# Optimization experiments

Hardware: AMD Instinct MI355X
Metric: run time of the kernel (lower is better)

The kernel has to match this reference:

```python
import jax, jax.numpy as jnp
import numpy as np

B, NPG, DIN, ED, DEG = 16, 1024, 16, 8, 32
HEADS, OUT1 = 5, 6
HID = HEADS * OUT1          # 30 features after conv1
C1, C2 = 32, 4              # DIFFPool cluster counts
N = B * NPG                 # 16384 total nodes
E = N * DEG                 # 524288 edges


def _egat_conv(x, src, dst, eattr, W, a_s, a_d, We, heads, outc, n_nodes):
    # Edge-gated GAT: per-edge attention logits from src/dst node features plus
    # a linear projection of edge attributes, segment-softmax over incoming edges.
    h = (x @ W).reshape(n_nodes, heads, outc)
    logit = jax.nn.leaky_relu((h[src] * a_s).sum(-1) + (h[dst] * a_d).sum(-1) + eattr @ We, 0.2)  # [E, heads]
    m = jax.ops.segment_max(logit, dst, num_segments=n_nodes)
    ex = jnp.exp(logit - m[dst])
    den = jax.ops.segment_sum(ex, dst, num_segments=n_nodes)
    alpha = ex / (den[dst] + 1e-16)
    out = jax.ops.segment_sum(alpha[:, :, None] * h[src], dst, num_segments=n_nodes)
    return out.reshape(n_nodes, heads * outc), alpha


def _diff_pool(x, adj, s_logits, b, n, c, d):
    s = jax.nn.softmax(s_logits.reshape(b, n, c), axis=-1)
    xp = jnp.einsum('bnc,bnd->bcd', s, x.reshape(b, n, d))
    adjp = jnp.einsum('bnc,bnm,bmk->bck', s, adj, s)
    reg = jnp.mean((adj - jnp.einsum('bnc,bmc->bnm', s, s)) ** 2)  # link-pred loss
    return xp.reshape(b * c, d), adjp, reg


def _dense_edges(b, c):
    base = jnp.arange(c)
    off = (jnp.arange(b) * c)[:, None]
    src = (jnp.repeat(base, c)[None, :] + off).reshape(-1)
    dst = (jnp.tile(base, c)[None, :] + off).reshape(-1)
    return src, dst


def _forward(x, edge_index, edge_attr, adj, params):
    (W1, a_src1, a_dst1, We1, Wp1, as_p1, ad_p1, Wep1,
     Wp2, as_p2, ad_p2, Wep2, Wf1, bf1, Wf2, bf2) = params
    src, dst = edge_index[0], edge_index[1]
    x1, e = _egat_conv(x, src, dst, edge_attr, W1, a_src1, a_dst1, We1, HEADS, OUT1, N)  # [N,30]
    e_dot = jnp.prod(e, axis=-1)[:, None]  # _EGATConv.dot: product over heads (unused downstream)
    s1, _ = _egat_conv(x1, src, dst, edge_attr, Wp1, as_p1, ad_p1, Wep1, 1, C1, N)
    x2, adj2, reg1 = _diff_pool(x1, adj, s1, B, NPG, C1, HID)
    src2, dst2 = _dense_edges(B, C1)
    ea2 = adj2.reshape(B * C1 * C1, 1)  # pooled graph is dense; adj values as edge attrs
    s2, _ = _egat_conv(x2, src2, dst2, ea2, Wp2, as_p2, ad_p2, Wep2, 1, C2, B * C1)
    x3, _, reg2 = _diff_pool(x2, adj2, s2, B, C1, C2, HID)
    reg = reg1 * 10.0 + reg2 * 0.1
    z = x3.reshape(B, C2 * HID)
    z = jax.nn.relu(z @ Wf1 + bf1)
    logits = z @ Wf2 + bf2
    return logits, reg


def setup_inputs() -> dict:
    key = jax.random.key(0)
    ks = jax.random.split(key, 20)
    # block-diagonal random edges: each graph has NPG*DEG edges within its block
    src_l = jax.random.randint(ks[0], (B, NPG * DEG), 0, NPG)
    dst_l = jax.random.randint(ks[1], (B, NPG * DEG), 0, NPG)
    off = (jnp.arange(B) * NPG)[:, None]
    edge_index = jnp.stack([(src_l + off).reshape(-1), (dst_l + off).reshape(-1)])
    adj = jnp.zeros((B, NPG, NPG), jnp.float32).at[jnp.arange(B)[:, None], src_l, dst_l].set(1.0)
    edge_attr = jax.random.uniform(ks[2], (E, ED), jnp.float32)
    x = jax.random.normal(ks[3], (N, DIN), jnp.float32)
    y = jax.random.randint(ks[4], (B,), 0, 2)

    def nrm(k, shape, fan):
        return jax.random.normal(k, shape, jnp.float32) / np.float32(np.sqrt(fan))

    return dict(
        x=x, edge_index=edge_index, edge_attr=edge_attr, y=y, adj=adj,
        W1=nrm(ks[5], (DIN, HEADS * OUT1), DIN),
        a_src1=nrm(ks[6], (HEADS, OUT1), OUT1),
        a_dst1=nrm(ks[7], (HEADS, OUT1), OUT1),
        We1=nrm(ks[8], (ED, HEADS), ED),
        Wp1=nrm(ks[9], (HID, C1), HID),
        as_p1=nrm(ks[10], (1, C1), C1),
        ad_p1=nrm(ks[11], (1, C1), C1),
        Wep1=nrm(ks[12], (ED, 1), ED),
        Wp2=nrm(ks[13], (HID, C2), HID),
        as_p2=nrm(ks[14], (1, C2), C2),
        ad_p2=nrm(ks[15], (1, C2), C2),
        Wep2=nrm(ks[16], (1, 1), 1),
        Wf1=nrm(ks[17], (C2 * HID, 32), C2 * HID),
        bf1=jnp.zeros((32,), jnp.float32),
        Wf2=nrm(ks[18], (32, 2), 32),
        bf2=jnp.zeros((2,), jnp.float32),
    )


def reference(x, edge_index, edge_attr, y, adj, W1, a_src1, a_dst1, We1, Wp1, as_p1, ad_p1, Wep1, Wp2, as_p2, ad_p2, Wep2, Wf1, bf1, Wf2, bf2):
    params = (W1, a_src1, a_dst1, We1, Wp1, as_p1, ad_p1, Wep1,
              Wp2, as_p2, ad_p2, Wep2, Wf1, bf1, Wf2, bf2)
    return _forward(x, edge_index, edge_attr, adj, params)
```

## Files before the change

kernel.cpp:

```cpp
#include <hip/hip_runtime.h>
#include <math.h>

#define NB 16
#define NPG 1024
#define DIN 16
#define ED 8
#define NHEADS 5
#define OUT1 6
#define HID 30
#define C1 32
#define C2 4
#define NN (NB*NPG)
#define EE (NN*32)
#define EPG 32768
#define CH 16
#define CE 2048

__device__ __forceinline__ float lrelu(float v){ return v >= 0.f ? v : 0.2f*v; }

__device__ __forceinline__ void chunk_gc(int& g, int& c){
    int x = blockIdx.x & 7;
    int j = blockIdx.x >> 3;
    g = x + 8*(j >> 4);
    c = j & 15;
}

__device__ __forceinline__ size_t xcd_chunk_base(){
    int x = blockIdx.x & 7;
    int j = blockIdx.x >> 3;
    int g = x + 8*(j >> 7);
    int c = j & 127;
    return (size_t)g*EPG + (size_t)c*256;
}

__global__ void k_hist_chunk(const int* __restrict__ src, const int* __restrict__ dst,
                             int* __restrict__ histD, int* __restrict__ histS,
                             const float* __restrict__ x, const float* __restrict__ W1,
                             const float* __restrict__ as1, const float* __restrict__ ad1,
                             float* __restrict__ h1, float* __restrict__ hs1, float* __restrict__ hd1){
    int t = threadIdx.x;
    if (blockIdx.x < 256){
        __shared__ int hD[NPG], hS[NPG];
        for (int i = t; i < NPG; i += 256){ hD[i] = 0; hS[i] = 0; }
        __syncthreads();
        int g, c; chunk_gc(g, c);
        size_t e0 = ((size_t)g*CH + c)*CE;
        #pragma unroll
        for (int i = 0; i < 8; i++){
            size_t e = e0 + i*256 + t;
            atomicAdd(&hD[dst[e] & (NPG-1)], 1);
            atomicAdd(&hS[src[e] & (NPG-1)], 1);
        }
        __syncthreads();
        size_t hb = ((size_t)g*CH + c)*NPG;
        for (int i = t; i < NPG; i += 256){
            histD[hb + i] = hD[i];
            histS[hb + i] = hS[i];
        }
        return;
    }
    __shared__ float Ws[DIN*HID];
    __shared__ float as_s[HID], ad_s[HID];
    for (int i = t; i < DIN*HID; i += blockDim.x) Ws[i] = W1[i];
    if (t < HID){ as_s[t] = as1[t]; ad_s[t] = ad1[t]; }
    __syncthreads();
    int n = (blockIdx.x - 256)*blockDim.x + t;
    if (n >= NN) return;
    float xv[DIN];
    #pragma unroll
    for (int i = 0; i < DIN; i++) xv[i] = x[n*DIN + i];
    float hv[HID];
    #pragma unroll
    for (int j = 0; j < HID; j++){
        float a = 0.f;
        #pragma unroll
        for (int i = 0; i < DIN; i++) a += xv[i]*Ws[i*HID + j];
        hv[j] = a; h1[(size_t)n*HID + j] = a;
    }
    #pragma unroll
    for (int h = 0; h < NHEADS; h++){
        float s = 0.f, d = 0.f;
        #pragma unroll
        for (int c2 = 0; c2 < OUT1; c2++){ s += hv[h*OUT1+c2]*as_s[h*OUT1+c2]; d += hv[h*OUT1+c2]*ad_s[h*OUT1+c2]; }
        hs1[n*NHEADS + h] = s; hd1[n*NHEADS + h] = d;
    }
}

__global__ __launch_bounds__(1024) void k_cumscan(int* __restrict__ histD, int* __restrict__ histS,
                                                  int* __restrict__ rowptr, int* __restrict__ rowptrS){
    __shared__ int wtot[16], wbase[16];
    bool isD = (blockIdx.x < NB);
    int b = isD ? blockIdx.x : (blockIdx.x - NB);
    int* hist = isD ? histD : histS;
    int* rp   = isD ? rowptr : rowptrS;
    int n = threadIdx.x;
    int run = 0;
    #pragma unroll
    for (int c = 0; c < CH; c++){
        size_t idx = ((size_t)b*CH + c)*NPG + n;
        int v = hist[idx];
        hist[idx] = run;
        run += v;
    }
    int lane = n & 63, wv = n >> 6;
    int sincl = run;
    #pragma unroll
    for (int off = 1; off < 64; off <<= 1){
        int v = __shfl_up(sincl, off, 64);
        if (lane >= off) sincl += v;
    }
    if (lane == 63) wtot[wv] = sincl;
    __syncthreads();
    if (n == 0){
        int r = 0;
        #pragma unroll
        for (int w = 0; w < 16; w++){ wbase[w] = r; r += wtot[w]; }
    }
    __syncthreads();
    int excl = wbase[wv] + sincl - run;
    rp[b*NPG + n] = b*EPG + excl;
    if (b == NB-1 && n == NPG-1) rp[NN] = EE;
}

__global__ void k_scatter_det(const int* __restrict__ src, const int* __restrict__ dst,
                              const int* __restrict__ rowptr, const int* __restrict__ rowptrS,
                              const int* __restrict__ histD, const int* __restrict__ histS,
                              int* __restrict__ srcs, int* __restrict__ eid,
                              int* __restrict__ dsts, int* __restrict__ nbrS){
    __shared__ int baseD[NPG], baseS[NPG];
    int t = threadIdx.x;
    int g, c; chunk_gc(g, c);
    size_t hb = ((size_t)g*CH + c)*NPG;
    for (int i = t; i < NPG; i += 256){
        baseD[i] = rowptr[g*NPG + i] + histD[hb + i];
        baseS[i] = rowptrS[g*NPG + i] + histS[hb + i];
    }
    __syncthreads();
    size_t e0 = ((size_t)g*CH + c)*CE;
    #pragma unroll
    for (int i = 0; i < 8; i++){
        size_t e = e0 + i*256 + t;
        int s = src[e], d = dst[e];
        int p = atomicAdd(&baseD[d & (NPG-1)], 1);
        srcs[p] = s; eid[p] = (int)e; dsts[p] = d;
        int pS = atomicAdd(&baseS[s & (NPG-1)], 1);
        nbrS[pS] = d;
    }
}

__global__ void k_elogit(const float* __restrict__ ea, const float* __restrict__ We1,
                         const float* __restrict__ Wep1,
                         const int* __restrict__ srcs, const int* __restrict__ eid,
                         const int* __restrict__ dsts,
                         const float* __restrict__ hs1, const float* __restrict__ hd1,
                         float* __restrict__ lg1T, float* __restrict__ ewp1s){
    __shared__ float W[ED*NHEADS];
    __shared__ float Wp[ED];
    int t = threadIdx.x;
    if (t < ED*NHEADS) W[t] = We1[t];
    if (t < ED) Wp[t] = Wep1[t];
    __syncthreads();
    size_t k = xcd_chunk_base() + t;
    int s = srcs[k], e = eid[k], d = dsts[k];
    float a[ED];
    #pragma unroll
    for (int i = 0; i < ED; i++) a[i] = ea[(size_t)e*ED + i];
    const float* hsr = hs1 + (size_t)s*NHEADS;
    const float* hdr = hd1 + (size_t)d*NHEADS;
    #pragma unroll
    for (int h = 0; h < NHEADS; h++){
        float sv = 0.f;
        #pragma unroll
        for (int i = 0; i < ED; i++) sv += a[i]*W[i*NHEADS + h];
        lg1T[(size_t)h*EE + k] = lrelu(hsr[h] + hdr[h] + sv);
    }
    float sv = 0.f;
    #pragma unroll
    for (int i = 0; i < ED; i++) sv += a[i]*Wp[i];
    ewp1s[k] = sv;
}

__global__ __launch_bounds__(640) void k_conv1_agg(const int* __restrict__ srcs,
                            const int* __restrict__ rowptr,
                            const float* __restrict__ h1, const float* __restrict__ lg1T,
                            float* __restrict__ x1){
    __shared__ float hls[NPG*HID];
    int t = threadIdx.x;
    int xx = blockIdx.x & 7;
    int j = blockIdx.x >> 3;
    int g = xx + 8*(j >> 4);
    int seg = j & 15;
    const float* hg = h1 + (size_t)g*NPG*HID;
    for (int i = t; i < NPG*HID; i += 640) hls[i] = hg[i];
    __syncthreads();
    int nl = seg*64 + t/10;
    int r = t - (t/10)*10;
    int h = r >> 1;
    int q = r & 1;
    int n = g*NPG + nl;
    int k0 = rowptr[n], k1 = rowptr[n+1];
    const float* lgh = lg1T + (size_t)h*EE;
    int off = h*OUT1 + q*3;
    float m = -INFINITY, den = 0.f;
    float acc[3] = {0.f, 0.f, 0.f};
    int k = k0;
    for (; k + 4 <= k1; k += 4){
        float l0 = lgh[k+0], l1 = lgh[k+1], l2 = lgh[k+2], l3 = lgh[k+3];
        int s0 = srcs[k+0] & (NPG-1), s1 = srcs[k+1] & (NPG-1);
        int s2 = srcs[k+2] & (NPG-1), s3 = srcs[k+3] & (NPG-1);
        const float* p0 = hls + s0*HID + off;
        const float* p1 = hls + s1*HID + off;
        const float* p2 = hls + s2*HID + off;
        const float* p3 = hls + s3*HID + off;
        float mb = fmaxf(fmaxf(l0, l1), fmaxf(l2, l3));
        float mn = fmaxf(m, mb);
        float f  = expf(m - mn);
        float e0 = expf(l0 - mn), e1 = expf(l1 - mn);
        float e2 = expf(l2 - mn), e3 = expf(l3 - mn);
        m = mn;
        den = den*f + e0 + e1 + e2 + e3;
        #pragma unroll
        for (int c = 0; c < 3; c++)
            acc[c] = acc[c]*f + e0*p0[c] + e1*p1[c] + e2*p2[c] + e3*p3[c];
    }
    for (; k < k1; k++){
        float l = lgh[k];
        int s = srcs[k] & (NPG-1);
        float mn = fmaxf(m, l);
        float f  = expf(m - mn);
        float ex = expf(l - mn);
        m = mn;
        den = den*f + ex;
        const float* hr = hls + s*HID + off;
        #pragma unroll
        for (int c = 0; c < 3; c++) acc[c] = acc[c]*f + ex*hr[c];
    }
    float inv = 1.f / (den + 1e-16f);
    #pragma unroll
    for (int c = 0; c < 3; c++) x1[(size_t)n*HID + off + c] = acc[c]*inv;
}

__global__ void k_pd(const float* __restrict__ x1, const float* __restrict__ Wp1,
                     const float* __restrict__ asp, const float* __restrict__ adp,
                     float* __restrict__ hp1, float* __restrict__ hsp, float* __restrict__ hdp,
                     const int* __restrict__ rowptrS, const int* __restrict__ nbrS,
                     int* __restrict__ unbr, int* __restrict__ ucnt,
                     float* __restrict__ scal){
    __shared__ float Ws[HID*C1];
    __shared__ float as_s[C1], ad_s[C1];
    __shared__ unsigned int bm[256*33];
    __shared__ int red[256];
    int t = threadIdx.x;
    if (blockIdx.x < 64){
        for (int i = t; i < HID*C1; i += blockDim.x) Ws[i] = Wp1[i];
        if (t < C1){ as_s[t] = asp[t]; ad_s[t] = adp[t]; }
        __syncthreads();
        int n = blockIdx.x*blockDim.x + t;
        float xv[HID];
        #pragma unroll
        for (int d = 0; d < HID; d++) xv[d] = x1[(size_t)n*HID + d];
        float s = 0.f, dd = 0.f;
        for (int c = 0; c < C1; c++){
            float a = 0.f;
            #pragma unroll
            for (int d = 0; d < HID; d++) a += xv[d]*Ws[d*C1 + c];
            hp1[(size_t)n*C1 + c] = a;
            s += a*as_s[c]; dd += a*ad_s[c];
        }
        hsp[n] = s; hdp[n] = dd;
        return;
    }
    unsigned int* mybm = &bm[t*33];
    #pragma unroll
    for (int i = 0; i < 32; i++) mybm[i] = 0u;
    int n = (blockIdx.x - 64)*blockDim.x + t;
    int cnt = 0;
    {
        int k0 = rowptrS[n], k1 = rowptrS[n+1];
        for (int k = k0; k < k1; k++){
            int m = nbrS[k];
            int loc = m & (NPG-1);
            unsigned int w = (unsigned int)(loc >> 5);
            unsigned int bit = 1u << (loc & 31);
            unsigned int old = mybm[w];
            if (!(old & bit)){
                mybm[w] = old | bit;
                unbr[k0 + cnt] = m;
                cnt++;
            }
        }
        ucnt[n] = cnt;
    }
    red[t] = cnt; __syncthreads();
    for (int s = 128; s > 0; s >>= 1){ if (t < s) red[t] += red[t+s]; __syncthreads(); }
    if (t == 0) atomicAdd(&scal[0], (float)red[0]);
}

__global__ void k_plogit(const int* __restrict__ srcs, const int* __restrict__ dsts,
                         const float* __restrict__ hsp, const float* __restrict__ hdp,
                         const float* __restrict__ ewp1s, float* __restrict__ lgp){
    size_t k = xcd_chunk_base() + threadIdx.x;
    lgp[k] = lrelu(hsp[srcs[k]] + hdp[dsts[k]] + ewp1s[k]);
}

__global__ void k_pool1_agg(const int* __restrict__ srcs, const int* __restrict__ rowptr,
                            const float* __restrict__ hp1, const float* __restrict__ lgp,
                            float* __restrict__ ssoft){
    __shared__ float sm[16*33];
    int tid = blockIdx.x*blockDim.x + threadIdx.x;
    int r = tid & 15;
    int q = r >> 1;
    int eh = r & 1;
    int n = tid >> 4;
    int nl = threadIdx.x >> 4;
    int k0 = rowptr[n], k1 = rowptr[n+1];
    int mid = k0 + ((k1 - k0 + 1) >> 1);
    int ka = eh ? mid : k0;
    int kb = eh ? k1 : mid;
    float m = -INFINITY, den = 0.f;
    float acc[4] = {0.f, 0.f, 0.f, 0.f};
    int k = ka;
    for (; k + 4 <= kb; k += 4){
        float l0 = lgp[k+0], l1 = lgp[k+1], l2 = lgp[k+2], l3 = lgp[k+3];
        int s0 = srcs[k+0], s1n = srcs[k+1], s2 = srcs[k+2], s3 = srcs[k+3];
        float4 v0 = *(const float4*)(hp1 + (size_t)s0*C1 + q*4);
        float4 v1 = *(const float4*)(hp1 + (size_t)s1n*C1 + q*4);
        float4 v2 = *(const float4*)(hp1 + (size_t)s2*C1 + q*4);
        float4 v3 = *(const float4*)(hp1 + (size_t)s3*C1 + q*4);
        float mb = fmaxf(fmaxf(l0, l1), fmaxf(l2, l3));
        float mn = fmaxf(m, mb);
        float f  = expf(m - mn);
        float e0 = expf(l0 - mn), e1 = expf(l1 - mn);
        float e2 = expf(l2 - mn), e3 = expf(l3 - mn);
        m = mn;
        den = den*f + e0 + e1 + e2 + e3;
        acc[0] = acc[0]*f + e0*v0.x + e1*v1.x + e2*v2.x + e3*v3.x;
        acc[1] = acc[1]*f + e0*v0.y + e1*v1.y + e2*v2.y + e3*v3.y;
        acc[2] = acc[2]*f + e0*v0.z + e1*v1.z + e2*v2.z + e3*v3.z;
        acc[3] = acc[3]*f + e0*v0.w + e1*v1.w + e2*v2.w + e3*v3.w;
    }
    for (; k < kb; k++){
        float l = lgp[k];
        int s = srcs[k];
        float mn = fmaxf(m, l);
        float f  = expf(m - mn);
        float ex = expf(l - mn);
        m = mn;
        den = den*f + ex;
        const float* hr = hp1 + (size_t)s*C1 + q*4;
        #pragma unroll
        for (int c = 0; c < 4; c++) acc[c] = acc[c]*f + ex*hr[c];
    }
    float mo  = __shfl_xor(m, 1, 64);
    float dno = __shfl_xor(den, 1, 64);
    float ao[4];
    #pragma unroll
    for (int c = 0; c < 4; c++) ao[c] = __shfl_xor(acc[c], 1, 64);
    float M = fmaxf(m, mo);
    float f1 = (m  == -INFINITY) ? 0.f : expf(m  - M);
    float f2 = (mo == -INFINITY) ? 0.f : expf(mo - M);
    float DEN = den*f1 + dno*f2;
    if (eh == 0){
        float inv = 1.f / (DEN + 1e-16f);
        #pragma unroll
        for (int c = 0; c < 4; c++) sm[nl*33 + q*4 + c] = (acc[c]*f1 + ao[c]*f2)*inv;
    }
    __syncthreads();
    float mx = -INFINITY;
    #pragma unroll 8
    for (int i = 0; i < C1; i++) mx = fmaxf(mx, sm[nl*33 + i]);
    float sum = 0.f;
    #pragma unroll 8
    for (int i = 0; i < C1; i++) sum += expf(sm[nl*33 + i] - mx);
    float is = 1.f/sum;
    if (eh == 0){
        #pragma unroll
        for (int c = 0; c < 4; c++)
            ssoft[(size_t)n*C1 + q*4 + c] = expf(sm[nl*33 + q*4 + c] - mx)*is;
    }
}

__global__ void k_T(const int* __restrict__ rowptrS, const int* __restrict__ unbr,
                    const int* __restrict__ ucnt, const float* __restrict__ ssoft,
                    float* __restrict__ T){
    int tid = blockIdx.x*blockDim.x + threadIdx.x;
    int r = tid & 15;
    int q = r >> 1;
    int eh = r & 1;
    int n = tid >> 4;
    int k0 = rowptrS[n];
    int cnt = ucnt[n];
    int half = (cnt + 1) >> 1;
    int ia = eh ? half : 0;
    int ib = eh ? cnt : half;
    float acc[4] = {0.f, 0.f, 0.f, 0.f};
    int i = ia;
    for (; i + 4 <= ib; i += 4){
        int m0 = unbr[k0+i+0], m1 = unbr[k0+i+1], m2 = unbr[k0+i+2], m3 = unbr[k0+i+3];
        float4 v0 = *(const float4*)(ssoft + (size_t)m0*C1 + q*4);
        float4 v1 = *(const float4*)(ssoft + (size_t)m1*C1 + q*4);
        float4 v2 = *(const float4*)(ssoft + (size_t)m2*C1 + q*4);
        float4 v3 = *(const float4*)(ssoft + (size_t)m3*C1 + q*4);
        acc[0] += v0.x + v1.x + v2.x + v3.x;
        acc[1] += v0.y + v1.y + v2.y + v3.y;
        acc[2] += v0.z + v1.z + v2.z + v3.z;
        acc[3] += v0.w + v1.w + v2.w + v3.w;
    }
    for (; i < ib; i++){
        int m = unbr[k0 + i];
        const float* sr = ssoft + (size_t)m*C1 + q*4;
        #pragma unroll
        for (int c = 0; c < 4; c++) acc[c] += sr[c];
    }
    #pragma unroll
    for (int c = 0; c < 4; c++) acc[c] += __shfl_xor(acc[c], 1, 64);
    if (eh == 0){
        #pragma unroll
        for (int c = 0; c < 4; c++) T[(size_t)n*C1 + q*4 + c] = acc[c];
    }
}

__global__ void k_partials(const float* __restrict__ ssoft, const float* __restrict__ T,
                           const float* __restrict__ x1,
                           float* __restrict__ adj2, float* __restrict__ Gm,
                           float* __restrict__ x2){
    int b  = blockIdx.y;
    int n0 = blockIdx.x * 64;
    int t  = threadIdx.x;
    __shared__ float ssh[64*C1];
    __shared__ float tsh[64*C1];
    __shared__ float xsh[64*HID];
    {
        size_t sbase = ((size_t)b*NPG + n0)*C1;
        #pragma unroll
        for (int i = 0; i < 8; i++){
            int lin = t + i*256;
            ssh[lin] = ssoft[sbase + lin];
            tsh[lin] = T[sbase + lin];
        }
        size_t xbase = ((size_t)b*NPG + n0)*HID;
        for (int lin = t; lin < 64*HID; lin += 256) xsh[lin] = x1[xbase + lin];
    }
    __syncthreads();
    float accA[4] = {0,0,0,0}, accG[4] = {0,0,0,0}, accX[4] = {0,0,0,0};
    int cA[4], kA[4], cX[4], dX[4];
    #pragma unroll
    for (int q = 0; q < 4; q++){
        int p = t + q*256;
        cA[q] = p >> 5; kA[q] = p & 31;
        cX[q] = p / HID; dX[q] = p - cX[q]*HID;
    }
    for (int r = 0; r < 64; r++){
        const float* sr = ssh + r*C1;
        const float* tr = tsh + r*C1;
        const float* xr = xsh + r*HID;
        #pragma unroll
        for (int q = 0; q < 4; q++){
            float sc = sr[cA[q]];
            accA[q] += sc*tr[kA[q]];
            accG[q] += sc*sr[kA[q]];
        }
        #pragma unroll
        for (int q = 0; q < 4; q++){
            int p = t + q*256;
            if (p < C1*HID) accX[q] += sr[cX[q]]*xr[dX[q]];
        }
    }
    #pragma unroll
    for (int q = 0; q < 4; q++){
        int p = t + q*256;
        atomicAdd(&adj2[(size_t)b*1024 + p], accA[q]);
        atomicAdd(&Gm[(size_t)b*1024 + p], accG[q]);
        if (p < C1*HID) atomicAdd(&x2[((size_t)b*C1 + cX[q])*HID + dX[q]], accX[q]);
    }
}

__global__ void k_tail(const float* __restrict__ x2, const float* __restrict__ adj2,
                       const float* __restrict__ Gm,
                       const float* __restrict__ Wp2, const float* __restrict__ asp,
                       const float* __restrict__ adp, const float* __restrict__ Wep2,
                       const float* __restrict__ Wf1, const float* __restrict__ bf1,
                       const float* __restrict__ Wf2, const float* __restrict__ bf2,
                       float* __restrict__ out, float* __restrict__ scal,
                       unsigned int* __restrict__ ctr){
    int b = blockIdx.x;
    int t = threadIdx.x;
    __shared__ float x2s[C1*HID];
    __shared__ float a2s[C1*C1];
    __shared__ float Wps[HID*C2];
    __shared__ float h2s[C1*C2];
    __shared__ float hs2s[C1], hd2s[C1];
    __shared__ float sss[C1*C2];
    __shared__ float x3s[C2*HID];
    __shared__ float zsh[32];
    __shared__ float red[256];
    for (int i = t; i < C1*HID; i += 256) x2s[i] = x2[(size_t)b*C1*HID + i];
    for (int i = t; i < C1*C1; i += 256) a2s[i] = adj2[(size_t)b*C1*C1 + i];
    if (t < HID*C2) Wps[t] = Wp2[t];
    __syncthreads();
    {
        float ltr = 0.f, lfr = 0.f;
        for (int p = t; p < 1024; p += 256){
            float g = Gm[(size_t)b*1024 + p];
            lfr += g*g;
            if ((p >> 5) == (p & 31)) ltr += a2s[p];
        }
        red[t] = ltr; __syncthreads();
        for (int s = 128; s > 0; s >>= 1){ if (t < s) red[t] += red[t+s]; __syncthreads(); }
        if (t == 0) atomicAdd(&scal[1], red[0]);
        __syncthreads();
        red[t] = lfr; __syncthreads();
        for (int s = 128; s > 0; s >>= 1){ if (t < s) red[t] += red[t+s]; __syncthreads(); }
        if (t == 0) atomicAdd(&scal[2], red[0]);
        __syncthreads();
    }
    if (t < C1){
        float s = 0.f, dd = 0.f;
        #pragma unroll
        for (int c = 0; c < C2; c++){
            float a = 0.f;
            #pragma unroll
            for (int d = 0; d < HID; d++) a += x2s[t*HID + d]*Wps[d*C2 + c];
            h2s[t*C2 + c] = a;
            s += a*asp[c]; dd += a*adp[c];
        }
        hs2s[t] = s; hd2s[t] = dd;
    }
    __syncthreads();
    if (t < C1){
        int j = t;
        float hdv = hd2s[j];
        float wep = Wep2[0];
        float m = -INFINITY;
        for (int i = 0; i < C1; i++)
            m = fmaxf(m, lrelu(hs2s[i] + hdv + a2s[i*C1 + j]*wep));
        float den = 0.f;
        float acc[C2] = {0,0,0,0};
        for (int i = 0; i < C1; i++){
            float ex = expf(lrelu(hs2s[i] + hdv + a2s[i*C1 + j]*wep) - m);
            den += ex;
            #pragma unroll
            for (int c = 0; c < C2; c++) acc[c] += ex * h2s[i*C2 + c];
        }
        float inv = 1.f/(den + 1e-16f);
        float v[C2]; float mx = -INFINITY;
        #pragma unroll
        for (int c = 0; c < C2; c++){ v[c] = acc[c]*inv; mx = fmaxf(mx, v[c]); }
        float sum = 0.f;
        #pragma unroll
        for (int c = 0; c < C2; c++){ v[c] = expf(v[c] - mx); sum += v[c]; }
        float i2 = 1.f/sum;
        #pragma unroll
        for (int c = 0; c < C2; c++) sss[j*C2 + c] = v[c]*i2;
    }
    __syncthreads();
    if (t < C2*HID){
        int c = t / HID, d = t % HID;
        float a = 0.f;
        #pragma unroll
        for (int n = 0; n < C1; n++) a += sss[n*C2 + c]*x2s[n*HID + d];
        x3s[t] = a;
    }
    {
        float loc = 0.f;
        for (int p = t; p < 1024; p += 256){
            int n = p >> 5, mm = p & 31;
            float dot = 0.f;
            #pragma unroll
            for (int c = 0; c < C2; c++) dot += sss[n*C2 + c]*sss[mm*C2 + c];
            float df = a2s[p] - dot;
            loc += df*df;
        }
        red[t] = loc; __syncthreads();
        for (int s = 128; s > 0; s >>= 1){ if (t < s) red[t] += red[t+s]; __syncthreads(); }
        if (t == 0) atomicAdd(&scal[3], red[0]);
        __syncthreads();
    }
    if (t < 32){
        float a = bf1[t];
        #pragma unroll 4
        for (int k = 0; k < C2*HID; k++) a += x3s[k]*Wf1[k*32 + t];
        zsh[t] = fmaxf(a, 0.f);
    }
    __syncthreads();
    if (t < 2){
        float a = bf2[t];
        #pragma unroll
        for (int j = 0; j < 32; j++) a += zsh[j]*Wf2[j*2 + t];
        out[b*2 + t] = a;
    }
    if (t == 0){
        __threadfence();
        unsigned int old = atomicAdd(ctr, 1u);
        if (old == NB - 1){
            float adjsum = atomicAdd(&scal[0], 0.f);
            float tr     = atomicAdd(&scal[1], 0.f);
            float fr     = atomicAdd(&scal[2], 0.f);
            float r2     = atomicAdd(&scal[3], 0.f);
            float reg1 = (adjsum - 2.f*tr + fr) * (1.f/16777216.f);
            float reg2 = r2 * (1.f/16384.f);
            out[32] = 10.f*reg1 + 0.1f*reg2;
        }
    }
}

extern "C" void kernel_launch(void* const* d_in, const int* in_sizes, int n_in,
                              void* d_out, int out_size, void* d_ws, size_t ws_size,
                              hipStream_t stream) {
    const float* x    = (const float*)d_in[0];
    const int*   ei   = (const int*)d_in[1];
    const float* ea   = (const float*)d_in[2];
    const float* W1   = (const float*)d_in[5];
    const float* as1  = (const float*)d_in[6];
    const float* ad1  = (const float*)d_in[7];
    const float* We1  = (const float*)d_in[8];
    const float* Wp1  = (const float*)d_in[9];
    const float* asp1 = (const float*)d_in[10];
    const float* adp1 = (const float*)d_in[11];
    const float* Wep1 = (const float*)d_in[12];
    const float* Wp2  = (const float*)d_in[13];
    const float* asp2 = (const float*)d_in[14];
    const float* adp2 = (const float*)d_in[15];
    const float* Wep2 = (const float*)d_in[16];
    const float* Wf1  = (const float*)d_in[17];
    const float* bf1  = (const float*)d_in[18];
    const float* Wf2  = (const float*)d_in[19];
    const float* bf2  = (const float*)d_in[20];
    float* out = (float*)d_out;

    const int* srcA = ei;
    const int* dstA = ei + EE;

    char* wp = (char*)d_ws;
    auto carve = [&](size_t bytes)->char*{
        char* p = wp;
        wp += (bytes + 255) & ~(size_t)255;
        return p;
    };
    float* h1    = (float*)carve((size_t)NN*HID*4);
    float* hs1   = (float*)carve((size_t)NN*NHEADS*4);
    float* hd1   = (float*)carve((size_t)NN*NHEADS*4);
    float* lg1T  = (float*)carve((size_t)EE*NHEADS*4);
    float* ewp1s = (float*)carve((size_t)EE*4);
    float* lgp   = (float*)carve((size_t)EE*4);
    float* x1    = (float*)carve((size_t)NN*HID*4);
    float* hp1   = (float*)carve((size_t)NN*C1*4);
    float* hsp   = (float*)carve((size_t)NN*4);
    float* hdp   = (float*)carve((size_t)NN*4);
    float* ssoft = (float*)carve((size_t)NN*C1*4);
    float* T     = (float*)carve((size_t)NN*C1*4);
    float* x2    = (float*)carve((size_t)NB*C1*HID*4);
    float* adj2  = (float*)carve((size_t)NB*C1*C1*4);
    float* Gm    = (float*)carve((size_t)NB*C1*C1*4);
    float* scal  = (float*)carve(16*4);
    unsigned int* ctr = (unsigned int*)(scal + 8);
    int* histD   = (int*)carve((size_t)NB*CH*NPG*4);
    int* histS   = (int*)carve((size_t)NB*CH*NPG*4);
    int* rowptr  = (int*)carve((size_t)(NN+1)*4);
    int* rowptrS = (int*)carve((size_t)(NN+1)*4);
    int* srcs    = (int*)carve((size_t)EE*4);
    int* eid     = (int*)carve((size_t)EE*4);
    int* dsts    = (int*)carve((size_t)EE*4);
    int* nbrS    = (int*)carve((size_t)EE*4);
    int* unbr    = (int*)carve((size_t)EE*4);
    int* ucnt    = (int*)carve((size_t)NN*4);

    hipMemsetAsync(scal, 0, 16*4, stream);
    hipMemsetAsync(x2, 0, (size_t)(NB*C1*HID + 2*NB*C1*C1)*4, stream);

    const int TB = 256;

    k_hist_chunk<<<dim3(256 + 64), TB, 0, stream>>>(srcA, dstA, histD, histS,
                                                    x, W1, as1, ad1, h1, hs1, hd1);
    k_cumscan<<<dim3(2*NB), 1024, 0, stream>>>(histD, histS, rowptr, rowptrS);
    k_scatter_det<<<dim3(256), TB, 0, stream>>>(srcA, dstA, rowptr, rowptrS,
                                                histD, histS, srcs, eid, dsts, nbrS);

    k_elogit<<<dim3(2048), TB, 0, stream>>>(ea, We1, Wep1, srcs, eid, dsts, hs1, hd1, lg1T, ewp1s);

    k_conv1_agg<<<dim3(256), 640, 0, stream>>>(srcs, rowptr, h1, lg1T, x1);

    k_pd<<<dim3(128), TB, 0, stream>>>(x1, Wp1, asp1, adp1, hp1, hsp, hdp,
                                       rowptrS, nbrS, unbr, ucnt, scal);

    k_plogit<<<dim3(2048), TB, 0, stream>>>(srcs, dsts, hsp, hdp, ewp1s, lgp);
    k_pool1_agg<<<dim3(NN*16/TB), TB, 0, stream>>>(srcs, rowptr, hp1, lgp, ssoft);

    k_T<<<dim3(NN*16/TB), TB, 0, stream>>>(rowptrS, unbr, ucnt, ssoft, T);
    k_partials<<<dim3(16, NB), TB, 0, stream>>>(ssoft, T, x1, adj2, Gm, x2);

    k_tail<<<dim3(NB), TB, 0, stream>>>(x2, adj2, Gm, Wp2, asp2, adp2, Wep2,
                                        Wf1, bf1, Wf2, bf2, out, scal, ctr);
}
```

Measured before the change: 280.2 us.

## Stage per-graph features in LDS for pool1 aggregation and neighbor-sum kernels

```diff
diff --git a/kernel.cpp b/kernel.cpp
--- a/kernel.cpp
+++ b/kernel.cpp
@@ -303,30 +303,35 @@
     lgp[k] = lrelu(hsp[srcs[k]] + hdp[dsts[k]] + ewp1s[k]);
 }
 
-__global__ void k_pool1_agg(const int* __restrict__ srcs, const int* __restrict__ rowptr,
+__global__ __launch_bounds__(512) void k_pool1_agg(const int* __restrict__ srcs,
+                            const int* __restrict__ rowptr,
                             const float* __restrict__ hp1, const float* __restrict__ lgp,
                             float* __restrict__ ssoft){
-    __shared__ float sm[16*33];
-    int tid = blockIdx.x*blockDim.x + threadIdx.x;
-    int r = tid & 15;
-    int q = r >> 1;
-    int eh = r & 1;
-    int n = tid >> 4;
-    int nl = threadIdx.x >> 4;
+    __shared__ float hls[NPG*33];
+    __shared__ float sm[64*33];
+    int t = threadIdx.x;
+    int xx = blockIdx.x & 7;
+    int j = blockIdx.x >> 3;
+    int g = xx + 8*(j >> 4);
+    int seg = j & 15;
+    const float* hg = hp1 + (size_t)g*NPG*C1;
+    for (int i = t; i < NPG*C1; i += 512){
+        int s = i >> 5, c = i & 31;
+        hls[s*33 + c] = hg[i];
+    }
+    __syncthreads();
+    int nl = t >> 3, q = t & 7;
+    int n = g*NPG + seg*64 + nl;
     int k0 = rowptr[n], k1 = rowptr[n+1];
-    int mid = k0 + ((k1 - k0 + 1) >> 1);
-    int ka = eh ? mid : k0;
-    int kb = eh ? k1 : mid;
     float m = -INFINITY, den = 0.f;
     float acc[4] = {0.f, 0.f, 0.f, 0.f};
-    int k = ka;
-    for (; k + 4 <= kb; k += 4){
+    int k = k0;
+    for (; k + 4 <= k1; k += 4){
         float l0 = lgp[k+0], l1 = lgp[k+1], l2 = lgp[k+2], l3 = lgp[k+3];
-        int s0 = srcs[k+0], s1n = srcs[k+1], s2 = srcs[k+2], s3 = srcs[k+3];
-        float4 v0 = *(const float4*)(hp1 + (size_t)s0*C1 + q*4);
-        float4 v1 = *(const float4*)(hp1 + (size_t)s1n*C1 + q*4);
-        float4 v2 = *(const float4*)(hp1 + (size_t)s2*C1 + q*4);
-        float4 v3 = *(const float4*)(hp1 + (size_t)s3*C1 + q*4);
+        int b0 = (srcs[k+0] & (NPG-1))*33 + q*4;
+        int b1 = (srcs[k+1] & (NPG-1))*33 + q*4;
+        int b2 = (srcs[k+2] & (NPG-1))*33 + q*4;
+        int b3 = (srcs[k+3] & (NPG-1))*33 + q*4;
         float mb = fmaxf(fmaxf(l0, l1), fmaxf(l2, l3));
         float mn = fmaxf(m, mb);
         float f  = expf(m - mn);
@@ -334,37 +339,24 @@
         float e2 = expf(l2 - mn), e3 = expf(l3 - mn);
         m = mn;
         den = den*f + e0 + e1 + e2 + e3;
-        acc[0] = acc[0]*f + e0*v0.x + e1*v1.x + e2*v2.x + e3*v3.x;
-        acc[1] = acc[1]*f + e0*v0.y + e1*v1.y + e2*v2.y + e3*v3.y;
-        acc[2] = acc[2]*f + e0*v0.z + e1*v1.z + e2*v2.z + e3*v3.z;
-        acc[3] = acc[3]*f + e0*v0.w + e1*v1.w + e2*v2.w + e3*v3.w;
-    }
-    for (; k < kb; k++){
+        #pragma unroll
+        for (int c = 0; c < 4; c++)
+            acc[c] = acc[c]*f + e0*hls[b0+c] + e1*hls[b1+c] + e2*hls[b2+c] + e3*hls[b3+c];
+    }
+    for (; k < k1; k++){
         float l = lgp[k];
-        int s = srcs[k];
+        int b = (srcs[k] & (NPG-1))*33 + q*4;
         float mn = fmaxf(m, l);
         float f  = expf(m - mn);
         float ex = expf(l - mn);
         m = mn;
         den = den*f + ex;
-        const float* hr = hp1 + (size_t)s*C1 + q*4;
-        #pragma unroll
-        for (int c = 0; c < 4; c++) acc[c] = acc[c]*f + ex*hr[c];
-    }
-    float mo  = __shfl_xor(m, 1, 64);
-    float dno = __shfl_xor(den, 1, 64);
-    float ao[4];
-    #pragma unroll
-    for (int c = 0; c < 4; c++) ao[c] = __shfl_xor(acc[c], 1, 64);
-    float M = fmaxf(m, mo);
-    float f1 = (m  == -INFINITY) ? 0.f : expf(m  - M);
-    float f2 = (mo == -INFINITY) ? 0.f : expf(mo - M);
-    float DEN = den*f1 + dno*f2;
-    if (eh == 0){
-        float inv = 1.f / (DEN + 1e-16f);
-        #pragma unroll
-        for (int c = 0; c < 4; c++) sm[nl*33 + q*4 + c] = (acc[c]*f1 + ao[c]*f2)*inv;
-    }
+        #pragma unroll
+        for (int c = 0; c < 4; c++) acc[c] = acc[c]*f + ex*hls[b+c];
+    }
+    float inv = 1.f / (den + 1e-16f);
+    #pragma unroll
+    for (int c = 0; c < 4; c++) sm[nl*33 + q*4 + c] = acc[c]*inv;
     __syncthreads();
     float mx = -INFINITY;
     #pragma unroll 8
@@ -373,51 +365,49 @@
     #pragma unroll 8
     for (int i = 0; i < C1; i++) sum += expf(sm[nl*33 + i] - mx);
     float is = 1.f/sum;
-    if (eh == 0){
-        #pragma unroll
-        for (int c = 0; c < 4; c++)
-            ssoft[(size_t)n*C1 + q*4 + c] = expf(sm[nl*33 + q*4 + c] - mx)*is;
-    }
-}
-
-__global__ void k_T(const int* __restrict__ rowptrS, const int* __restrict__ unbr,
+    #pragma unroll
+    for (int c = 0; c < 4; c++)
+        ssoft[(size_t)n*C1 + q*4 + c] = expf(sm[nl*33 + q*4 + c] - mx)*is;
+}
+
+__global__ __launch_bounds__(512) void k_T(const int* __restrict__ rowptrS,
+                    const int* __restrict__ unbr,
                     const int* __restrict__ ucnt, const float* __restrict__ ssoft,
                     float* __restrict__ T){
-    int tid = blockIdx.x*blockDim.x + threadIdx.x;
-    int r = tid & 15;
-    int q = r >> 1;
-    int eh = r & 1;
-    int n = tid >> 4;
+    __shared__ float sls[NPG*33];
+    int t = threadIdx.x;
+    int xx = blockIdx.x & 7;
+    int j = blockIdx.x >> 3;
+    int g = xx + 8*(j >> 4);
+    int seg = j & 15;
+    const float* sg = ssoft + (size_t)g*NPG*C1;
+    for (int i = t; i < NPG*C1; i += 512){
+        int s = i >> 5, c = i & 31;
+        sls[s*33 + c] = sg[i];
+    }
+    __syncthreads();
+    int nl = t >> 3, q = t & 7;
+    int n = g*NPG + seg*64 + nl;
     int k0 = rowptrS[n];
     int cnt = ucnt[n];
-    int half = (cnt + 1) >> 1;
-    int ia = eh ? half : 0;
-    int ib = eh ? cnt : half;
     float acc[4] = {0.f, 0.f, 0.f, 0.f};
-    int i = ia;
-    for (; i + 4 <= ib; i += 4){
-        int m0 = unbr[k0+i+0], m1 = unbr[k0+i+1], m2 = unbr[k0+i+2], m3 = unbr[k0+i+3];
-        float4 v0 = *(const float4*)(ssoft + (size_t)m0*C1 + q*4);
-        float4 v1 = *(const float4*)(ssoft + (size_t)m1*C1 + q*4);
-        float4 v2 = *(const float4*)(ssoft + (size_t)m2*C1 + q*4);
-        float4 v3 = *(const float4*)(ssoft + (size_t)m3*C1 + q*4);
-        acc[0] += v0.x + v1.x + v2.x + v3.x;
-        acc[1] += v0.y + v1.y + v2.y + v3.y;
-        acc[2] += v0.z + v1.z + v2.z + v3.z;
-        acc[3] += v0.w + v1.w + v2.w + v3.w;
-    }
-    for (; i < ib; i++){
-        int m = unbr[k0 + i];
-        const float* sr = ssoft + (size_t)m*C1 + q*4;
-        #pragma unroll
-        for (int c = 0; c < 4; c++) acc[c] += sr[c];
-    }
-    #pragma unroll
-    for (int c = 0; c < 4; c++) acc[c] += __shfl_xor(acc[c], 1, 64);
-    if (eh == 0){
-        #pragma unroll
-        for (int c = 0; c < 4; c++) T[(size_t)n*C1 + q*4 + c] = acc[c];
-    }
+    int i = 0;
+    for (; i + 4 <= cnt; i += 4){
+        int b0 = (unbr[k0+i+0] & (NPG-1))*33 + q*4;
+        int b1 = (unbr[k0+i+1] & (NPG-1))*33 + q*4;
+        int b2 = (unbr[k0+i+2] & (NPG-1))*33 + q*4;
+        int b3 = (unbr[k0+i+3] & (NPG-1))*33 + q*4;
+        #pragma unroll
+        for (int c = 0; c < 4; c++)
+            acc[c] += sls[b0+c] + sls[b1+c] + sls[b2+c] + sls[b3+c];
+    }
+    for (; i < cnt; i++){
+        int b = (unbr[k0+i] & (NPG-1))*33 + q*4;
+        #pragma unroll
+        for (int c = 0; c < 4; c++) acc[c] += sls[b+c];
+    }
+    #pragma unroll
+    for (int c = 0; c < 4; c++) T[(size_t)n*C1 + q*4 + c] = acc[c];
 }
 
 __global__ void k_partials(const float* __restrict__ ssoft, const float* __restrict__ T,
@@ -684,9 +674,9 @@
                                        rowptrS, nbrS, unbr, ucnt, scal);
 
     k_plogit<<<dim3(2048), TB, 0, stream>>>(srcs, dsts, hsp, hdp, ewp1s, lgp);
-    k_pool1_agg<<<dim3(NN*16/TB), TB, 0, stream>>>(srcs, rowptr, hp1, lgp, ssoft);
-
-    k_T<<<dim3(NN*16/TB), TB, 0, stream>>>(rowptrS, unbr, ucnt, ssoft, T);
+    k_pool1_agg<<<dim3(256), 512, 0, stream>>>(srcs, rowptr, hp1, lgp, ssoft);
+
+    k_T<<<dim3(256), 512, 0, stream>>>(rowptrS, unbr, ucnt, ssoft, T);
     k_partials<<<dim3(16, NB), TB, 0, stream>>>(ssoft, T, x1, adj2, Gm, x2);
 
     k_tail<<<dim3(NB), TB, 0, stream>>>(x2, adj2, Gm, Wp2, asp2, adp2, Wep2,
```

Result: no change. 277.8 us (-0.9%).
